# Kernel optimization log

Hardware: AMD Instinct MI355X
Metric: run time of the kernel (lower is better)

Reference implementation:

```python
import jax, jax.numpy as jnp
import numpy as np

N, IN_FEAT, OUT_FEAT = 8192, 512, 256
SLOPE = 0.1


def setup_inputs() -> dict:
    key = jax.random.key(0)
    k1, k2, k3, k4, k5 = jax.random.split(key, 5)
    doc = jax.random.normal(k1, (N, IN_FEAT), dtype=jnp.float32)
    W = jax.random.normal(k2, (IN_FEAT, OUT_FEAT), dtype=jnp.float32) * (1.0 / np.sqrt(IN_FEAT))
    W_b = jax.random.normal(k3, (OUT_FEAT,), dtype=jnp.float32) * 0.01
    a = jax.random.normal(k4, (2 * OUT_FEAT,), dtype=jnp.float32) * (1.0 / np.sqrt(2 * OUT_FEAT))
    a_b = jax.random.normal(k5, (1,), dtype=jnp.float32) * 0.01
    return {"doc": doc, "W": W, "W_b": W_b, "a": a, "a_b": a_b}


def reference(doc, W, W_b, a, a_b):
    # h = W(doc): [N, outFeat]
    h = doc @ W + W_b
    d = h.shape[-1]
    # aParams(cat(h_i, h_j)) = a1.h_i + a2.h_j + b  (avoids the O(N^2*2d) concat)
    a1, a2 = a[:d], a[d:]
    score = (h @ a1)[:, None] + (h @ a2)[None, :] + a_b[0]  # [N, N]
    score = jax.nn.leaky_relu(score, SLOPE)
    # adj=None path -> all-ones mask, the where() is a no-op
    att = jax.nn.softmax(score, axis=1)  # normalize over neighbors j
    out = jax.nn.leaky_relu(att @ h, SLOPE)  # [N, outFeat]
    return out, att
```

## Files before the change

### kernel.cpp

```cpp
#include <hip/hip_runtime.h>
#include <hip/hip_bf16.h>


typedef __attribute__((ext_vector_type(4))) float f32x4;
typedef __attribute__((ext_vector_type(8))) short short8;
typedef __attribute__((ext_vector_type(4))) unsigned short ushort4v;

#define SLOPE 0.1f
#define NROW 8192
#define DDIM 256

__device__ __forceinline__ float lrelu(float x){ return fmaxf(x, SLOPE * x); }

__device__ __forceinline__ unsigned short f2bf(float f){
  union { float f; unsigned u; } v; v.f = f;
  unsigned r = (v.u + 0x7fffu + ((v.u >> 16) & 1u)) >> 16;
  return (unsigned short)r;
}

__device__ __forceinline__ unsigned cvt_pk_bf16(float lo, float hi){
  unsigned r;
  asm("v_cvt_pk_bf16_f32 %0, %1, %2" : "=v"(r) : "v"(lo), "v"(hi));
  return r;
}

__global__ __launch_bounds__(256) void k_h(
    const float* __restrict__ doc, const float* __restrict__ W,
    const float* __restrict__ Wb, float* __restrict__ h,
    unsigned short* __restrict__ ht)
{
  __shared__ __align__(16) float At[16][68];
  __shared__ __align__(16) float Bs[16][68];
  const int t  = threadIdx.x;
  const int cb = blockIdx.x * 64;
  const int rb = blockIdx.y * 64;
  const int tx = t & 15, ty = t >> 4;

  float acc[4][4] = {};
  const int srow = t >> 2, skq = t & 3;
  const int bk = t >> 4, bc = t & 15;

  for (int kk = 0; kk < 512; kk += 16) {
    f32x4 av = *reinterpret_cast<const f32x4*>(doc + (size_t)(rb + srow) * 512 + kk + skq * 4);
    f32x4 wv = *reinterpret_cast<const f32x4*>(W + (size_t)(kk + bk) * 256 + cb + bc * 4);
    __syncthreads();
    At[skq * 4 + 0][srow] = av[0];
    At[skq * 4 + 1][srow] = av[1];
    At[skq * 4 + 2][srow] = av[2];
    At[skq * 4 + 3][srow] = av[3];
    *reinterpret_cast<f32x4*>(&Bs[bk][bc * 4]) = wv;
    __syncthreads();
#pragma unroll
    for (int k = 0; k < 16; ++k) {
      f32x4 a4 = *reinterpret_cast<const f32x4*>(&At[k][ty * 4]);
      f32x4 b4 = *reinterpret_cast<const f32x4*>(&Bs[k][tx * 4]);
#pragma unroll
      for (int i = 0; i < 4; ++i)
#pragma unroll
        for (int j = 0; j < 4; ++j)
          acc[i][j] = fmaf(a4[i], b4[j], acc[i][j]);
    }
  }

  float bias[4];
#pragma unroll
  for (int j = 0; j < 4; ++j) bias[j] = Wb[cb + tx * 4 + j];

#pragma unroll
  for (int i = 0; i < 4; ++i) {
    const int r = rb + ty * 4 + i;
    f32x4 o;
#pragma unroll
    for (int j = 0; j < 4; ++j) o[j] = acc[i][j] + bias[j];
    *reinterpret_cast<f32x4*>(h + (size_t)r * 256 + cb + tx * 4) = o;
  }
#pragma unroll
  for (int j = 0; j < 4; ++j) {
    const int c = cb + tx * 4 + j;
    ushort4v u;
#pragma unroll
    for (int i = 0; i < 4; ++i) u[i] = f2bf(acc[i][j] + bias[j]);
    *reinterpret_cast<ushort4v*>(ht + (size_t)c * 8192 + rb + ty * 4) = u;
  }
}

__global__ __launch_bounds__(256) void k_s12(
    const float* __restrict__ h, const float* __restrict__ a,
    float* __restrict__ s1, float* __restrict__ s2,
    float* __restrict__ e2, float* __restrict__ e02)
{
  const int t = threadIdx.x, w = t >> 6, l = t & 63;
  float a1[4], a2[4];
#pragma unroll
  for (int q = 0; q < 4; ++q) { a1[q] = a[l + q * 64]; a2[q] = a[256 + l + q * 64]; }
  const int rbase = blockIdx.x * 32 + w * 8;
  for (int rr = 0; rr < 8; ++rr) {
    const int r = rbase + rr;
    float v1 = 0.f, v2 = 0.f;
#pragma unroll
    for (int q = 0; q < 4; ++q) {
      float hv = h[(size_t)r * 256 + l + q * 64];
      v1 = fmaf(hv, a1[q], v1);
      v2 = fmaf(hv, a2[q], v2);
    }
#pragma unroll
    for (int off = 32; off > 0; off >>= 1) { v1 += __shfl_down(v1, off); v2 += __shfl_down(v2, off); }
    if (l == 0) {
      s1[r] = v1; s2[r] = v2;
      e2[r] = __expf(v2); e02[r] = __expf(SLOPE * v2);
    }
  }
}

__global__ __launch_bounds__(256) void k_z(
    const float* __restrict__ s1, const float* __restrict__ e2g,
    const float* __restrict__ e02g, const float* __restrict__ abp,
    float* __restrict__ rowinfo)
{
  __shared__ __align__(16) float es[8192];
  __shared__ __align__(16) float fs[8192];
  const int t = threadIdx.x;
  for (int i = t * 4; i < 8192; i += 1024) {
    *reinterpret_cast<f32x4*>(&es[i]) = *reinterpret_cast<const f32x4*>(e2g + i);
    *reinterpret_cast<f32x4*>(&fs[i]) = *reinterpret_cast<const f32x4*>(e02g + i);
  }
  __syncthreads();
  const int w = t >> 6, l = t & 63;
  const float ab = abp[0];
  const int rb = blockIdx.x * 16 + w * 4;
  float T[4], E1[4], E01[4];
#pragma unroll
  for (int rr = 0; rr < 4; ++rr) {
    const float s1a = s1[rb + rr] + ab;
    E1[rr] = __expf(s1a); E01[rr] = __expf(SLOPE * s1a); T[rr] = __expf(-s1a);
  }
  float zA[4] = {0.f,0.f,0.f,0.f}, zB[4] = {0.f,0.f,0.f,0.f};
  for (int i = l * 4; i < 8192; i += 256) {
    const f32x4 e = *reinterpret_cast<const f32x4*>(&es[i]);
    const f32x4 f = *reinterpret_cast<const f32x4*>(&fs[i]);
#pragma unroll
    for (int rr = 0; rr < 4; ++rr)
#pragma unroll
      for (int q = 0; q < 4; ++q) {
        const bool c = (e[q] >= T[rr]);
        zA[rr] += c ? e[q] : 0.f;
        zB[rr] += c ? 0.f : f[q];
      }
  }
#pragma unroll
  for (int rr = 0; rr < 4; ++rr) {
    float z = E1[rr] * zA[rr] + E01[rr] * zB[rr];
#pragma unroll
    for (int off = 32; off > 0; off >>= 1) z += __shfl_down(z, off);
    if (l == 0) {
      const float iz = 1.0f / z;
      f32x4 ri = (f32x4){E1[rr] * iz, E01[rr] * iz, T[rr], iz};
      *reinterpret_cast<f32x4*>(rowinfo + (size_t)(rb + rr) * 4) = ri;
    }
  }
}

__global__ __launch_bounds__(256, 4) void k_att(
    const float* __restrict__ rowinfo, const float* __restrict__ e2g,
    const float* __restrict__ e02g, const unsigned short* __restrict__ ht,
    float* __restrict__ att, float* __restrict__ part, int CHUNK)
{
  extern __shared__ __align__(16) char smem[];
  char* plsb  = smem;
  float* e2s  = reinterpret_cast<float*>(smem + 8192);
  float* e02s = e2s + CHUNK;

  const int t = threadIdx.x, w = t >> 6, l = t & 63;
  const int lr = l & 15, lg = l >> 4;
  const int kbase = blockIdx.x * CHUNK;
  const int rb = blockIdx.y * 64;

  for (int i = t * 4; i < CHUNK; i += 1024) {
    *reinterpret_cast<f32x4*>(e2s + i)  = *reinterpret_cast<const f32x4*>(e2g + kbase + i);
    *reinterpret_cast<f32x4*>(e02s + i) = *reinterpret_cast<const f32x4*>(e02g + kbase + i);
  }

  const int r8 = l >> 3, jc = l & 7;
  const int rowA = rb + w * 16 + r8;
  const int rowB = rowA + 8;
  const f32x4 riA = *reinterpret_cast<const f32x4*>(rowinfo + (size_t)rowA * 4);
  const f32x4 riB = *reinterpret_cast<const f32x4*>(rowinfo + (size_t)rowB * 4);
  const float E1zA = riA[0], E01zA = riA[1], TA = riA[2];
  const float E1zB = riB[0], E01zB = riB[1], TB = riB[2];
  float* attA = att + (size_t)rowA * 8192 + kbase + jc * 4;
  float* attB = att + (size_t)rowB * 8192 + kbase + jc * 4;
  const int fragA = w * 1024 + ((jc >> 1) * 16 + r8) * 16 + (jc & 1) * 8;
  const int fragB = fragA + 128;

  __syncthreads();

  auto gen = [&](int kw, int pb) {
    const f32x4 eA = *reinterpret_cast<const f32x4*>(e2s + kw + jc * 4);
    const f32x4 fA = *reinterpret_cast<const f32x4*>(e02s + kw + jc * 4);
    f32x4 pA, pB;
#pragma unroll
    for (int q = 0; q < 4; ++q) {
      const bool cA = (eA[q] >= TA);
      pA[q] = (cA ? E1zA : E01zA) * (cA ? eA[q] : fA[q]);
      const bool cB = (eA[q] >= TB);
      pB[q] = (cB ? E1zB : E01zB) * (cB ? eA[q] : fA[q]);
    }
    __builtin_nontemporal_store(pA, reinterpret_cast<f32x4*>(attA + kw));
    __builtin_nontemporal_store(pB, reinterpret_cast<f32x4*>(attB + kw));
    uint2 uA, uB;
    uA.x = cvt_pk_bf16(pA[0], pA[1]); uA.y = cvt_pk_bf16(pA[2], pA[3]);
    uB.x = cvt_pk_bf16(pB[0], pB[1]); uB.y = cvt_pk_bf16(pB[2], pB[3]);
    *reinterpret_cast<uint2*>(plsb + pb * 4096 + fragA) = uA;
    *reinterpret_cast<uint2*>(plsb + pb * 4096 + fragB) = uB;
  };

  f32x4 acc[4][4];
#pragma unroll
  for (int rt = 0; rt < 4; ++rt)
#pragma unroll
    for (int ct = 0; ct < 4; ++ct) acc[rt][ct] = (f32x4){0.f, 0.f, 0.f, 0.f};

  const unsigned short* hbase = ht + (size_t)(w * 64 + lr) * 8192 + kbase + lg * 8;

  gen(0, 0);

  const int NIT = CHUNK / 32;
  for (int n = 0; n < NIT; ++n) {
    const int kk = n * 32;
    const int par = n & 1;

    asm volatile("s_waitcnt lgkmcnt(0)\n\ts_barrier" ::: "memory");

    const short8 b0 = *reinterpret_cast<const short8*>(hbase + kk);
    const short8 b1 = *reinterpret_cast<const short8*>(hbase + kk + (size_t)16 * 8192);
    const short8 b2 = *reinterpret_cast<const short8*>(hbase + kk + (size_t)32 * 8192);
    const short8 b3 = *reinterpret_cast<const short8*>(hbase + kk + (size_t)48 * 8192);

    const short8* pbuf = reinterpret_cast<const short8*>(plsb + par * 4096);
    const short8 af0 = pbuf[0 * 64 + l];
    const short8 af1 = pbuf[1 * 64 + l];
    const short8 af2 = pbuf[2 * 64 + l];
    const short8 af3 = pbuf[3 * 64 + l];

    if (n + 1 < NIT) gen(kk + 32, par ^ 1);

    __builtin_amdgcn_s_setprio(1);
    acc[0][0] = __builtin_amdgcn_mfma_f32_16x16x32_bf16(af0, b0, acc[0][0], 0, 0, 0);
    acc[1][0] = __builtin_amdgcn_mfma_f32_16x16x32_bf16(af1, b0, acc[1][0], 0, 0, 0);
    acc[2][0] = __builtin_amdgcn_mfma_f32_16x16x32_bf16(af2, b0, acc[2][0], 0, 0, 0);
    acc[3][0] = __builtin_amdgcn_mfma_f32_16x16x32_bf16(af3, b0, acc[3][0], 0, 0, 0);
    acc[0][1] = __builtin_amdgcn_mfma_f32_16x16x32_bf16(af0, b1, acc[0][1], 0, 0, 0);
    acc[1][1] = __builtin_amdgcn_mfma_f32_16x16x32_bf16(af1, b1, acc[1][1], 0, 0, 0);
    acc[2][1] = __builtin_amdgcn_mfma_f32_16x16x32_bf16(af2, b1, acc[2][1], 0, 0, 0);
    acc[3][1] = __builtin_amdgcn_mfma_f32_16x16x32_bf16(af3, b1, acc[3][1], 0, 0, 0);
    acc[0][2] = __builtin_amdgcn_mfma_f32_16x16x32_bf16(af0, b2, acc[0][2], 0, 0, 0);
    acc[1][2] = __builtin_amdgcn_mfma_f32_16x16x32_bf16(af1, b2, acc[1][2], 0, 0, 0);
    acc[2][2] = __builtin_amdgcn_mfma_f32_16x16x32_bf16(af2, b2, acc[2][2], 0, 0, 0);
    acc[3][2] = __builtin_amdgcn_mfma_f32_16x16x32_bf16(af3, b2, acc[3][2], 0, 0, 0);
    acc[0][3] = __builtin_amdgcn_mfma_f32_16x16x32_bf16(af0, b3, acc[0][3], 0, 0, 0);
    acc[1][3] = __builtin_amdgcn_mfma_f32_16x16x32_bf16(af1, b3, acc[1][3], 0, 0, 0);
    acc[2][3] = __builtin_amdgcn_mfma_f32_16x16x32_bf16(af2, b3, acc[2][3], 0, 0, 0);
    acc[3][3] = __builtin_amdgcn_mfma_f32_16x16x32_bf16(af3, b3, acc[3][3], 0, 0, 0);
    __builtin_amdgcn_s_setprio(0);
  }

  float* pb = part + (size_t)blockIdx.x * ((size_t)NROW * DDIM);
#pragma unroll
  for (int rt = 0; rt < 4; ++rt)
#pragma unroll
    for (int ct = 0; ct < 4; ++ct)
#pragma unroll
      for (int q = 0; q < 4; ++q)
        __builtin_nontemporal_store(acc[rt][ct][q],
            pb + (size_t)(rb + rt * 16 + lg * 4 + q) * 256 + w * 64 + ct * 16 + lr);
}

__global__ __launch_bounds__(256) void k_reduce(
    const float* __restrict__ part, float* __restrict__ out, int KS)
{
  const size_t idx = ((size_t)blockIdx.x * 256 + threadIdx.x) * 4;
  f32x4 s = __builtin_nontemporal_load(reinterpret_cast<const f32x4*>(part + idx));
  for (int k = 1; k < KS; ++k) {
    const f32x4 v = __builtin_nontemporal_load(
        reinterpret_cast<const f32x4*>(part + (size_t)k * NROW * DDIM + idx));
#pragma unroll
    for (int q = 0; q < 4; ++q) s[q] += v[q];
  }
#pragma unroll
  for (int q = 0; q < 4; ++q) s[q] = lrelu(s[q]);
  __builtin_nontemporal_store(s, reinterpret_cast<f32x4*>(out + idx));
}

extern "C" void kernel_launch(void* const* d_in, const int* in_sizes, int n_in,
                              void* d_out, int out_size, void* d_ws, size_t ws_size,
                              hipStream_t stream)
{
  const float* doc = (const float*)d_in[0];
  const float* W   = (const float*)d_in[1];
  const float* Wb  = (const float*)d_in[2];
  const float* a   = (const float*)d_in[3];
  const float* ab  = (const float*)d_in[4];

  float* out = (float*)d_out;
  float* att = out + (size_t)8192 * 256;

  char* ws = (char*)d_ws;
  float* h           = (float*)ws;
  unsigned short* ht = (unsigned short*)(ws + (size_t)8 * 1024 * 1024);
  char* tb           = ws + (size_t)12 * 1024 * 1024;
  float* s1  = (float*)tb;
  float* s2  = s1 + 8192;
  float* e2  = s2 + 8192;
  float* e02 = e2 + 8192;
  float* rowinfo = e02 + 8192;
  const size_t base = (size_t)12 * 1024 * 1024 + 288 * 1024;
  const size_t partBytes = (size_t)NROW * DDIM * sizeof(float);

  int KS = 1;
  for (int c = 8; c >= 1; c >>= 1)
    if (base + (size_t)c * partBytes <= ws_size) { KS = c; break; }
  float* part = (float*)(ws + base);
  const int CHUNK = NROW / KS;
  const size_t smem = 8192 + (size_t)2 * CHUNK * sizeof(float);

  hipLaunchKernelGGL(k_h,      dim3(4, 128),   dim3(256), 0,    stream, doc, W, Wb, h, ht);
  hipLaunchKernelGGL(k_s12,    dim3(256),      dim3(256), 0,    stream, h, a, s1, s2, e2, e02);
  hipLaunchKernelGGL(k_z,      dim3(512),      dim3(256), 0,    stream, s1, e2, e02, ab, rowinfo);
  hipLaunchKernelGGL(k_att,    dim3(KS, 128),  dim3(256), smem, stream, rowinfo, e2, e02, ht, att, part, CHUNK);
  hipLaunchKernelGGL(k_reduce, dim3(2048),     dim3(256), 0,    stream, part, out, KS);
}
```

Measured before the change: 153.1 us.

## Compute projection with split-bf16 MFMA and fuse score dot products into it

Replaces the fp32 SIMT tiled GEMM for h = doc@W with bf16 MFMA, splitting W and doc into hi/lo bf16 parts (three MFMAs per tile) to keep near-fp32 accuracy. A new prep kernel transposes and splits W. The s1/s2 attention-projection reduction is fused into the GEMM epilogue, so the separate k_s12 kernel and the fp32 h buffer disappear and only bf16 ht is written. It also caps the split-K partition count at 4. The cost is an extra kernel launch and three times the MFMA work. Precision is slightly lower than the fp32 path.

```diff
diff --git a/kernel.cpp b/kernel.cpp
--- a/kernel.cpp
+++ b/kernel.cpp
@@ -17,98 +17,166 @@
   unsigned r = (v.u + 0x7fffu + ((v.u >> 16) & 1u)) >> 16;
   return (unsigned short)r;
 }
-
+__device__ __forceinline__ float bf2f(unsigned short u){
+  union { unsigned u; float f; } v; v.u = (unsigned)u << 16; return v.f;
+}
 __device__ __forceinline__ unsigned cvt_pk_bf16(float lo, float hi){
   unsigned r;
   asm("v_cvt_pk_bf16_f32 %0, %1, %2" : "=v"(r) : "v"(lo), "v"(hi));
   return r;
 }
 
+__global__ __launch_bounds__(256) void k_prep(
+    const float* __restrict__ W,
+    unsigned short* __restrict__ Wt_hi, unsigned short* __restrict__ Wt_lo)
+{
+  const int tid = blockIdx.x * 256 + threadIdx.x;
+  const int c = tid >> 7, kq = tid & 127;
+  ushort4v hi, lo;
+#pragma unroll
+  for (int j = 0; j < 4; ++j) {
+    const float v = W[(size_t)(kq * 4 + j) * 256 + c];
+    hi[j] = f2bf(v);
+    lo[j] = f2bf(v - bf2f(hi[j]));
+  }
+  *reinterpret_cast<ushort4v*>(Wt_hi + (size_t)c * 512 + kq * 4) = hi;
+  *reinterpret_cast<ushort4v*>(Wt_lo + (size_t)c * 512 + kq * 4) = lo;
+}
+
 __global__ __launch_bounds__(256) void k_h(
-    const float* __restrict__ doc, const float* __restrict__ W,
-    const float* __restrict__ Wb, float* __restrict__ h,
-    unsigned short* __restrict__ ht)
-{
-  __shared__ __align__(16) float At[16][68];
-  __shared__ __align__(16) float Bs[16][68];
-  const int t  = threadIdx.x;
-  const int cb = blockIdx.x * 64;
-  const int rb = blockIdx.y * 64;
-  const int tx = t & 15, ty = t >> 4;
-
-  float acc[4][4] = {};
-  const int srow = t >> 2, skq = t & 3;
-  const int bk = t >> 4, bc = t & 15;
-
-  for (int kk = 0; kk < 512; kk += 16) {
-    f32x4 av = *reinterpret_cast<const f32x4*>(doc + (size_t)(rb + srow) * 512 + kk + skq * 4);
-    f32x4 wv = *reinterpret_cast<const f32x4*>(W + (size_t)(kk + bk) * 256 + cb + bc * 4);
-    __syncthreads();
-    At[skq * 4 + 0][srow] = av[0];
-    At[skq * 4 + 1][srow] = av[1];
-    At[skq * 4 + 2][srow] = av[2];
-    At[skq * 4 + 3][srow] = av[3];
-    *reinterpret_cast<f32x4*>(&Bs[bk][bc * 4]) = wv;
-    __syncthreads();
-#pragma unroll
-    for (int k = 0; k < 16; ++k) {
-      f32x4 a4 = *reinterpret_cast<const f32x4*>(&At[k][ty * 4]);
-      f32x4 b4 = *reinterpret_cast<const f32x4*>(&Bs[k][tx * 4]);
-#pragma unroll
-      for (int i = 0; i < 4; ++i)
-#pragma unroll
-        for (int j = 0; j < 4; ++j)
-          acc[i][j] = fmaf(a4[i], b4[j], acc[i][j]);
+    const float* __restrict__ doc, const unsigned short* __restrict__ Wt_hi,
+    const unsigned short* __restrict__ Wt_lo, const float* __restrict__ Wb,
+    const float* __restrict__ a,
+    unsigned short* __restrict__ ht, float* __restrict__ s1,
+    float* __restrict__ e2, float* __restrict__ e02)
+{
+  __shared__ __align__(16) short8 aH[2][2][64];
+  __shared__ __align__(16) short8 aL[2][2][64];
+  __shared__ float sred[4][2][32];
+
+  const int t = threadIdx.x, w = t >> 6, l = t & 63;
+  const int lr = l & 15, lg = l >> 4;
+  const int rb = blockIdx.x * 32;
+  const int cb = w * 64;
+
+  f32x4 acc[2][4];
+#pragma unroll
+  for (int rt = 0; rt < 2; ++rt)
+#pragma unroll
+    for (int ct = 0; ct < 4; ++ct) acc[rt][ct] = (f32x4){0.f, 0.f, 0.f, 0.f};
+
+  const float* docp = doc + (size_t)(rb + w * 16 + lr) * 512 + lg * 8;
+
+  f32x4 v0, v1;
+  auto loadDoc = [&](int k0) { if (w < 2) {
+      v0 = *reinterpret_cast<const f32x4*>(docp + k0);
+      v1 = *reinterpret_cast<const f32x4*>(docp + k0 + 4);
+  }};
+  auto writeStage = [&](int pb) { if (w < 2) {
+      union { short8 v; unsigned short u[8]; } hi, lo;
+#pragma unroll
+      for (int q = 0; q < 4; ++q) {
+        hi.u[q] = f2bf(v0[q]);     lo.u[q] = f2bf(v0[q] - bf2f(hi.u[q]));
+        hi.u[4+q] = f2bf(v1[q]);   lo.u[4+q] = f2bf(v1[q] - bf2f(hi.u[4+q]));
+      }
+      aH[pb][w][l] = hi.v;
+      aL[pb][w][l] = lo.v;
+  }};
+
+  loadDoc(0); writeStage(0); loadDoc(32);
+
+  for (int n = 0; n < 16; ++n) {
+    const int kk = n * 32;
+    const int par = n & 1;
+
+    asm volatile("s_waitcnt lgkmcnt(0)\n\ts_barrier" ::: "memory");
+
+    const short8 ah0 = aH[par][0][l];
+    const short8 ah1 = aH[par][1][l];
+    const short8 al0 = aL[par][0][l];
+    const short8 al1 = aL[par][1][l];
+
+    short8 bh[4], bl[4];
+#pragma unroll
+    for (int ct = 0; ct < 4; ++ct) {
+      const size_t off = (size_t)(cb + ct * 16 + lr) * 512 + kk + lg * 8;
+      bh[ct] = *reinterpret_cast<const short8*>(Wt_hi + off);
+      bl[ct] = *reinterpret_cast<const short8*>(Wt_lo + off);
+    }
+
+    if (n + 1 < 16) writeStage(par ^ 1);
+    if (n + 2 < 16) loadDoc((n + 2) * 32);
+
+#pragma unroll
+    for (int ct = 0; ct < 4; ++ct) {
+      acc[0][ct] = __builtin_amdgcn_mfma_f32_16x16x32_bf16(ah0, bh[ct], acc[0][ct], 0, 0, 0);
+      acc[1][ct] = __builtin_amdgcn_mfma_f32_16x16x32_bf16(ah1, bh[ct], acc[1][ct], 0, 0, 0);
+      acc[0][ct] = __builtin_amdgcn_mfma_f32_16x16x32_bf16(ah0, bl[ct], acc[0][ct], 0, 0, 0);
+      acc[1][ct] = __builtin_amdgcn_mfma_f32_16x16x32_bf16(ah1, bl[ct], acc[1][ct], 0, 0, 0);
+      acc[0][ct] = __builtin_amdgcn_mfma_f32_16x16x32_bf16(al0, bh[ct], acc[0][ct], 0, 0, 0);
+      acc[1][ct] = __builtin_amdgcn_mfma_f32_16x16x32_bf16(al1, bh[ct], acc[1][ct], 0, 0, 0);
     }
   }
 
   float bias[4];
 #pragma unroll
-  for (int j = 0; j < 4; ++j) bias[j] = Wb[cb + tx * 4 + j];
-
-#pragma unroll
-  for (int i = 0; i < 4; ++i) {
-    const int r = rb + ty * 4 + i;
-    f32x4 o;
-#pragma unroll
-    for (int j = 0; j < 4; ++j) o[j] = acc[i][j] + bias[j];
-    *reinterpret_cast<f32x4*>(h + (size_t)r * 256 + cb + tx * 4) = o;
-  }
-#pragma unroll
-  for (int j = 0; j < 4; ++j) {
-    const int c = cb + tx * 4 + j;
-    ushort4v u;
-#pragma unroll
-    for (int i = 0; i < 4; ++i) u[i] = f2bf(acc[i][j] + bias[j]);
-    *reinterpret_cast<ushort4v*>(ht + (size_t)c * 8192 + rb + ty * 4) = u;
-  }
-}
-
-__global__ __launch_bounds__(256) void k_s12(
-    const float* __restrict__ h, const float* __restrict__ a,
-    float* __restrict__ s1, float* __restrict__ s2,
-    float* __restrict__ e2, float* __restrict__ e02)
-{
-  const int t = threadIdx.x, w = t >> 6, l = t & 63;
-  float a1[4], a2[4];
-#pragma unroll
-  for (int q = 0; q < 4; ++q) { a1[q] = a[l + q * 64]; a2[q] = a[256 + l + q * 64]; }
-  const int rbase = blockIdx.x * 32 + w * 8;
-  for (int rr = 0; rr < 8; ++rr) {
-    const int r = rbase + rr;
-    float v1 = 0.f, v2 = 0.f;
+  for (int ct = 0; ct < 4; ++ct) bias[ct] = Wb[cb + ct * 16 + lr];
+#pragma unroll
+  for (int rt = 0; rt < 2; ++rt)
+#pragma unroll
+    for (int ct = 0; ct < 4; ++ct) {
+#pragma unroll
+      for (int q = 0; q < 4; ++q) acc[rt][ct][q] += bias[ct];
+      ushort4v u;
+#pragma unroll
+      for (int q = 0; q < 4; ++q) u[q] = f2bf(acc[rt][ct][q]);
+      *reinterpret_cast<ushort4v*>(
+          ht + (size_t)(cb + ct * 16 + lr) * 8192 + rb + rt * 16 + lg * 4) = u;
+    }
+
+  float a1c[4], a2c[4];
+#pragma unroll
+  for (int ct = 0; ct < 4; ++ct) {
+    a1c[ct] = a[cb + ct * 16 + lr];
+    a2c[ct] = a[256 + cb + ct * 16 + lr];
+  }
+  float p1[2][4], p2[2][4];
+#pragma unroll
+  for (int rt = 0; rt < 2; ++rt)
 #pragma unroll
     for (int q = 0; q < 4; ++q) {
-      float hv = h[(size_t)r * 256 + l + q * 64];
-      v1 = fmaf(hv, a1[q], v1);
-      v2 = fmaf(hv, a2[q], v2);
-    }
-#pragma unroll
-    for (int off = 32; off > 0; off >>= 1) { v1 += __shfl_down(v1, off); v2 += __shfl_down(v2, off); }
-    if (l == 0) {
-      s1[r] = v1; s2[r] = v2;
-      e2[r] = __expf(v2); e02[r] = __expf(SLOPE * v2);
-    }
+      float x1 = 0.f, x2 = 0.f;
+#pragma unroll
+      for (int ct = 0; ct < 4; ++ct) {
+        x1 = fmaf(acc[rt][ct][q], a1c[ct], x1);
+        x2 = fmaf(acc[rt][ct][q], a2c[ct], x2);
+      }
+#pragma unroll
+      for (int off = 1; off < 16; off <<= 1) {
+        x1 += __shfl_xor(x1, off);
+        x2 += __shfl_xor(x2, off);
+      }
+      p1[rt][q] = x1; p2[rt][q] = x2;
+    }
+  __syncthreads();
+  if (lr == 0) {
+#pragma unroll
+    for (int rt = 0; rt < 2; ++rt)
+#pragma unroll
+      for (int q = 0; q < 4; ++q) {
+        sred[w][0][rt * 16 + lg * 4 + q] = p1[rt][q];
+        sred[w][1][rt * 16 + lg * 4 + q] = p2[rt][q];
+      }
+  }
+  __syncthreads();
+  if (t < 32) {
+    float v1s = 0.f, v2s = 0.f;
+#pragma unroll
+    for (int ww = 0; ww < 4; ++ww) { v1s += sred[ww][0][t]; v2s += sred[ww][1][t]; }
+    const int r = rb + t;
+    s1[r] = v1s;
+    e2[r] = __expf(v2s);
+    e02[r] = __expf(SLOPE * v2s);
   }
 }
 
@@ -305,27 +373,26 @@
   float* att = out + (size_t)8192 * 256;
 
   char* ws = (char*)d_ws;
-  float* h           = (float*)ws;
-  unsigned short* ht = (unsigned short*)(ws + (size_t)8 * 1024 * 1024);
-  char* tb           = ws + (size_t)12 * 1024 * 1024;
-  float* s1  = (float*)tb;
-  float* s2  = s1 + 8192;
-  float* e2  = s2 + 8192;
-  float* e02 = e2 + 8192;
+  unsigned short* ht    = (unsigned short*)ws;
+  unsigned short* Wt_hi = (unsigned short*)(ws + (size_t)4 * 1024 * 1024);
+  unsigned short* Wt_lo = Wt_hi + (size_t)256 * 512;
+  float* s1      = (float*)(ws + (size_t)4 * 1024 * 1024 + 512 * 1024);
+  float* e2      = s1 + 8192;
+  float* e02     = e2 + 8192;
   float* rowinfo = e02 + 8192;
-  const size_t base = (size_t)12 * 1024 * 1024 + 288 * 1024;
+  const size_t base = (size_t)5 * 1024 * 1024;
   const size_t partBytes = (size_t)NROW * DDIM * sizeof(float);
 
   int KS = 1;
-  for (int c = 8; c >= 1; c >>= 1)
+  for (int c = 4; c >= 1; c >>= 1)
     if (base + (size_t)c * partBytes <= ws_size) { KS = c; break; }
   float* part = (float*)(ws + base);
   const int CHUNK = NROW / KS;
   const size_t smem = 8192 + (size_t)2 * CHUNK * sizeof(float);
 
-  hipLaunchKernelGGL(k_h,      dim3(4, 128),   dim3(256), 0,    stream, doc, W, Wb, h, ht);
-  hipLaunchKernelGGL(k_s12,    dim3(256),      dim3(256), 0,    stream, h, a, s1, s2, e2, e02);
-  hipLaunchKernelGGL(k_z,      dim3(512),      dim3(256), 0,    stream, s1, e2, e02, ab, rowinfo);
-  hipLaunchKernelGGL(k_att,    dim3(KS, 128),  dim3(256), smem, stream, rowinfo, e2, e02, ht, att, part, CHUNK);
-  hipLaunchKernelGGL(k_reduce, dim3(2048),     dim3(256), 0,    stream, part, out, KS);
-}
+  hipLaunchKernelGGL(k_prep,   dim3(128),     dim3(256), 0,    stream, W, Wt_hi, Wt_lo);
+  hipLaunchKernelGGL(k_h,      dim3(256),     dim3(256), 0,    stream, doc, Wt_hi, Wt_lo, Wb, a, ht, s1, e2, e02);
+  hipLaunchKernelGGL(k_z,      dim3(512),     dim3(256), 0,    stream, s1, e2, e02, ab, rowinfo);
+  hipLaunchKernelGGL(k_att,    dim3(KS, 128), dim3(256), smem, stream, rowinfo, e2, e02, ht, att, part, CHUNK);
+  hipLaunchKernelGGL(k_reduce, dim3(2048),    dim3(256), 0,    stream, part, out, KS);
+}
```

New measurement: 145.7 us. 1.05x faster.
